# Kernel tuning notes

Measured on AMD Instinct MI355X. Metric: run time of the kernel, lower is better.

## Reference

```python
import jax, jax.numpy as jnp
import numpy as np

WS = 14           # window_size
N = WS * WS       # tokens = 196
DIM = 768
H = 12
HD = DIM // H     # 64
B = 256
KSZ = 3


def make_local_mask():
    # True = masked out; 3x3 neighborhood around each query is kept (False)
    mask = np.ones((N, N), dtype=bool)
    for i in range(WS):
        for j in range(WS):
            cur = np.ones((WS, WS), dtype=bool)
            stx, sty = max(i - KSZ // 2, 0), max(j - KSZ // 2, 0)
            edx, edy = min(i + KSZ // 2, WS - 1), min(j + KSZ // 2, WS - 1)
            cur[stx:edx + 1, sty:edy + 1] = False
            mask[i * WS + j] = cur.reshape(-1)
    return mask


def make_rel_idx():
    coords = np.stack(np.meshgrid(np.arange(WS), np.arange(WS), indexing='ij'))  # [2,WS,WS]
    flat = coords.reshape(2, -1)                                                  # [2,N]
    rel = flat[:, :, None] - flat[:, None, :]                                     # [2,N,N]
    rel = rel.transpose(1, 2, 0).astype(np.int32)                                 # [N,N,2]
    rel[:, :, 0] += WS - 1
    rel[:, :, 1] += WS - 1
    rel[:, :, 0] *= 2 * WS - 1
    return rel.sum(-1)                                                            # [N,N] in [0, (2WS-1)^2)


def setup_inputs() -> dict:
    key = jax.random.key(0)
    ks = jax.random.split(key, 5)
    return {
        'x': jax.random.normal(ks[0], (B, N, DIM), jnp.float32),
        'w_qkv': jax.random.normal(ks[1], (3 * DIM, DIM), jnp.float32) * 0.02,
        'rpb_table': jax.random.normal(ks[2], ((2 * WS - 1) ** 2, H), jnp.float32) * 0.02,
        'proj_w': jax.random.normal(ks[3], (DIM, DIM), jnp.float32) * 0.02,
        'proj_b': jax.random.normal(ks[4], (DIM,), jnp.float32) * 0.02,
        'mask': jnp.asarray(make_local_mask()),
        'rel_idx': jnp.asarray(make_rel_idx()),
    }


def reference(x, w_qkv, rpb_table, proj_w, proj_b, mask, rel_idx):
    b, n, c = x.shape
    scale = HD ** -0.5
    qkv = x @ w_qkv.T                                   # [B,N,3*DIM]
    qkv = qkv.reshape(b, n, 3, H, HD).transpose(2, 0, 3, 1, 4)  # [3,B,H,N,HD]
    q, k, v = qkv[0] * scale, qkv[1], qkv[2]
    attn = jnp.einsum('bhqd,bhkd->bhqk', q, k)          # [B,H,N,N]
    neg = -jnp.finfo(attn.dtype).max
    attn = jnp.where(mask, neg, attn)
    # relative position bias gather: [N,N] indices into [T,H] -> [H,N,N]
    rpb = rpb_table[rel_idx].transpose(2, 0, 1)
    attn = attn + rpb[None]
    attn = jax.nn.softmax(attn, axis=-1)
    out = jnp.einsum('bhqk,bhkd->bhqd', attn, v)        # [B,H,N,HD]
    out = out.transpose(0, 2, 1, 3).reshape(b, n, H * HD)
    return out @ proj_w.T + proj_b
```

## Files before the change

### kernel.cpp

```cpp
#include <hip/hip_runtime.h>
#include <cstdint>
#include <cstddef>

typedef unsigned short u16;
typedef __attribute__((ext_vector_type(8))) short bf16x8;
typedef __attribute__((ext_vector_type(4))) float f32x4;

__device__ __forceinline__ u16 f2bf(float f) {
    unsigned u = __float_as_uint(f);
    u += 0x7FFF + ((u >> 16) & 1);
    return (u16)(u >> 16);
}
__device__ __forceinline__ float bf2f(u16 b) {
    return __uint_as_float(((unsigned)b) << 16);
}

__global__ __launch_bounds__(256) void cvt_bf16(const float4* __restrict__ in,
                                                u16* __restrict__ out, int n4) {
    int i = blockIdx.x * 256 + threadIdx.x;
    if (i >= n4) return;
    float4 v = in[i];
    ushort4 o;
    o.x = f2bf(v.x); o.y = f2bf(v.y); o.z = f2bf(v.z); o.w = f2bf(v.w);
    ((ushort4*)out)[i] = o;
}

constexpr int BM = 128, BN = 128, BK = 32;

__device__ __forceinline__ void gl_lds16(const u16* g, u16* l) {
    __builtin_amdgcn_global_load_lds(
        (const __attribute__((address_space(1))) void*)g,
        (__attribute__((address_space(3))) void*)l, 16, 0, 0);
}

template <bool IS_QKV>
__global__ __launch_bounds__(256)
void gemm_bt(const u16* __restrict__ A, const u16* __restrict__ Bt,
             const float* __restrict__ bias, void* __restrict__ Cout,
             int M, int N, int K)
{
    __shared__ u16 As[BM * BK];
    __shared__ u16 Bs[BN * BK];

    const int tid  = threadIdx.x;
    const int wave = tid >> 6;
    const int lane = tid & 63;

    const int m0 = blockIdx.y * BM;
    const int n0 = blockIdx.x * BN;

    const int wm = (wave >> 1) * 64;
    const int wn = (wave & 1) * 64;

    const int fr = lane & 15;
    const int fks = (((lane >> 4) ^ ((fr >> 1) & 3)) * 8);

    f32x4 acc[4][4] = {};

    const int srow = wave * 32 + (lane >> 2);
    const int scol = (((lane & 3) ^ ((lane >> 3) & 3)) * 8);
    const u16* ag = A  + (size_t)(m0 + srow) * K + scol;
    const u16* bg = Bt + (size_t)(n0 + srow) * K + scol;
    u16* al0 = As + wave * 1024;
    u16* al1 = As + wave * 1024 + 512;
    u16* bl0 = Bs + wave * 1024;
    u16* bl1 = Bs + wave * 1024 + 512;

    for (int k0 = 0; k0 < K; k0 += BK) {
        gl_lds16(ag + k0,           al0);
        gl_lds16(ag + k0 + 16 * K,  al1);
        gl_lds16(bg + k0,           bl0);
        gl_lds16(bg + k0 + 16 * K,  bl1);
        __syncthreads();

        bf16x8 af[4], bfv[4];
        #pragma unroll
        for (int t = 0; t < 4; ++t) {
            af[t]  = *(const bf16x8*)(As + (wm + t * 16 + fr) * BK + fks);
            bfv[t] = *(const bf16x8*)(Bs + (wn + t * 16 + fr) * BK + fks);
        }
        #pragma unroll
        for (int tm = 0; tm < 4; ++tm)
            #pragma unroll
            for (int tn = 0; tn < 4; ++tn)
                acc[tm][tn] = __builtin_amdgcn_mfma_f32_16x16x32_bf16(
                    af[tm], bfv[tn], acc[tm][tn], 0, 0, 0);
        __syncthreads();
    }

    if (IS_QKV) {
        u16* C = (u16*)Cout;
        #pragma unroll
        for (int tm = 0; tm < 4; ++tm) {
            const int r0 = m0 + wm + tm * 16 + (lane >> 4) * 4;
            #pragma unroll
            for (int tn = 0; tn < 4; ++tn) {
                const int col = n0 + wn + tn * 16 + fr;
                const float sc = (col < 768) ? 0.125f : 1.0f;
                #pragma unroll
                for (int r = 0; r < 4; ++r)
                    C[(size_t)(r0 + r) * N + col] = f2bf(acc[tm][tn][r] * sc);
            }
        }
    } else {
        float* C = (float*)Cout;
        #pragma unroll
        for (int tm = 0; tm < 4; ++tm) {
            const int r0 = m0 + wm + tm * 16 + (lane >> 4) * 4;
            #pragma unroll
            for (int tn = 0; tn < 4; ++tn) {
                const int col = n0 + wn + tn * 16 + fr;
                const float b = bias[col];
                #pragma unroll
                for (int r = 0; r < 4; ++r)
                    C[(size_t)(r0 + r) * N + col] = acc[tm][tn][r] + b;
            }
        }
    }
}

__device__ __forceinline__ void load_bf8(const u16* p, float* f) {
    uint4 d = *(const uint4*)p;
    f[0] = __uint_as_float(d.x << 16); f[1] = __uint_as_float(d.x & 0xFFFF0000u);
    f[2] = __uint_as_float(d.y << 16); f[3] = __uint_as_float(d.y & 0xFFFF0000u);
    f[4] = __uint_as_float(d.z << 16); f[5] = __uint_as_float(d.z & 0xFFFF0000u);
    f[6] = __uint_as_float(d.w << 16); f[7] = __uint_as_float(d.w & 0xFFFF0000u);
}

__global__ __launch_bounds__(256)
void attn_sparse2(const u16* __restrict__ qkv, const float* __restrict__ rpb,
                  u16* __restrict__ out)
{
    const int lane = threadIdx.x & 63;
    const int wid  = blockIdx.x * 4 + (threadIdx.x >> 6);
    const int sub  = lane >> 3;
    const int sl   = lane & 7;
    const int gq   = wid * 8 + sub;
    const int bt   = gq / 12;
    const int h    = gq - bt * 12;
    const int t    = bt % 196;
    const int i    = t / 14, j = t % 14;

    const size_t rowbase = (size_t)(bt - t) * 2304 + h * 64 + sl * 8;

    float qf[8];
    load_bf8(qkv + (size_t)bt * 2304 + h * 64 + sl * 8, qf);

    float s[9];
    int   t2a[9];
    #pragma unroll
    for (int di = -1; di <= 1; ++di) {
        #pragma unroll
        for (int dj = -1; dj <= 1; ++dj) {
            const int idx = (di + 1) * 3 + (dj + 1);
            const int i2 = i + di, j2 = j + dj;
            const bool valid = ((unsigned)i2 < 14u) && ((unsigned)j2 < 14u);
            const int t2 = valid ? (i2 * 14 + j2) : t;
            t2a[idx] = t2;
            float kf[8];
            load_bf8(qkv + rowbase + (size_t)t2 * 2304 + 768, kf);
            float p = qf[0] * kf[0];
            #pragma unroll
            for (int d = 1; d < 8; ++d) p = fmaf(qf[d], kf[d], p);
            p += __shfl_xor(p, 1);
            p += __shfl_xor(p, 2);
            p += __shfl_xor(p, 4);
            const int ridx = (13 - di) * 27 + (13 - dj);
            s[idx] = valid ? (p + rpb[ridx * 12 + h]) : -1e30f;
        }
    }
    float mx = s[0];
    #pragma unroll
    for (int a = 1; a < 9; ++a) mx = fmaxf(mx, s[a]);

    float den = 0.f, o[8] = {};
    #pragma unroll
    for (int a = 0; a < 9; ++a) {
        float vf[8];
        load_bf8(qkv + rowbase + (size_t)t2a[a] * 2304 + 1536, vf);
        const float p = __expf(s[a] - mx);
        den += p;
        #pragma unroll
        for (int d = 0; d < 8; ++d) o[d] = fmaf(p, vf[d], o[d]);
    }
    const float r = 1.0f / den;
    ushort4 o0, o1;
    o0.x = f2bf(o[0] * r); o0.y = f2bf(o[1] * r);
    o0.z = f2bf(o[2] * r); o0.w = f2bf(o[3] * r);
    o1.x = f2bf(o[4] * r); o1.y = f2bf(o[5] * r);
    o1.z = f2bf(o[6] * r); o1.w = f2bf(o[7] * r);
    u16* op = out + (size_t)bt * 768 + h * 64 + sl * 8;
    *(ushort4*)op = o0;
    *(ushort4*)(op + 4) = o1;
}

extern "C" void kernel_launch(void* const* d_in, const int* in_sizes, int n_in,
                              void* d_out, int out_size, void* d_ws, size_t ws_size,
                              hipStream_t stream)
{
    const float* x      = (const float*)d_in[0];
    const float* w_qkv  = (const float*)d_in[1];
    const float* rpb    = (const float*)d_in[2];
    const float* proj_w = (const float*)d_in[3];
    const float* proj_b = (const float*)d_in[4];
    float* out = (float*)d_out;

    char* ws = (char*)d_ws;
    u16* x_bf    = (u16*)(ws);
    u16* wqkv_bf = (u16*)(ws + 77070336ULL);
    u16* pw_bf   = (u16*)(ws + 80609280ULL);
    u16* qkv_bf  = (u16*)(ws + 81788928ULL);
    u16* attn_bf = (u16*)(ws + 312999936ULL);

    cvt_bf16<<<37632, 256, 0, stream>>>((const float4*)x,      x_bf,    9633792);
    cvt_bf16<<<1728,  256, 0, stream>>>((const float4*)w_qkv,  wqkv_bf, 442368);
    cvt_bf16<<<576,   256, 0, stream>>>((const float4*)proj_w, pw_bf,   147456);

    gemm_bt<true><<<dim3(18, 392), 256, 0, stream>>>(
        x_bf, wqkv_bf, nullptr, qkv_bf, 50176, 2304, 768);

    attn_sparse2<<<18816, 256, 0, stream>>>(qkv_bf, rpb, attn_bf);

    gemm_bt<false><<<dim3(6, 392), 256, 0, stream>>>(
        attn_bf, pw_bf, proj_b, out, 50176, 768, 768);
}
```

Measured before the change: 756.4 us.

## Replace GEMM with 256x256 double-buffered pipelined MFMA kernel and XCD-aware tile remap

Swaps the 128x128 single-buffer GEMM for a 512-thread 256x256-tile kernel with BK=64 and double-buffered LDS. Global-to-LDS loads for the next k-step are interleaved with MFMA phases, and s_setprio raises priority during the MFMA runs. Block indices are remapped so neighbouring tiles land on the same XCD. The goal is to hide load latency and raise data reuse per tile, at the cost of more LDS and registers per block and fewer blocks in flight.

```diff
diff --git a/kernel.cpp b/kernel.cpp
--- a/kernel.cpp
+++ b/kernel.cpp
@@ -25,95 +25,174 @@
     ((ushort4*)out)[i] = o;
 }
 
-constexpr int BM = 128, BN = 128, BK = 32;
-
 __device__ __forceinline__ void gl_lds16(const u16* g, u16* l) {
     __builtin_amdgcn_global_load_lds(
         (const __attribute__((address_space(1))) void*)g,
         (__attribute__((address_space(3))) void*)l, 16, 0, 0);
 }
 
+#define MFMA16(a, b, c) __builtin_amdgcn_mfma_f32_16x16x32_bf16(a, b, c, 0, 0, 0)
+
+__device__ __forceinline__ void BARRIER() {
+    asm volatile("" ::: "memory");
+    __builtin_amdgcn_s_barrier();
+    asm volatile("" ::: "memory");
+}
+#define LGKM0() asm volatile("s_waitcnt lgkmcnt(0)" ::: "memory")
+
+__device__ __forceinline__ bf16x8 lds_frag(const u16* base, int r, int c) {
+    return *(const bf16x8*)((const char*)base + (r << 7) + ((c ^ (r & 7)) << 4));
+}
+
+__device__ __forceinline__ void stage_half(const u16* gbase, int K, u16* lbase,
+                                           int kt, int h, int srow, int wuoff)
+{
+    const u16* gp = gbase + (size_t)(h * 128 + srow) * K + kt * 64;
+    char* lp = (char*)lbase + h * 16384 + wuoff;
+    gl_lds16(gp, (u16*)lp);
+    gl_lds16(gp + (size_t)64 * K, (u16*)(lp + 8192));
+}
+
 template <bool IS_QKV>
-__global__ __launch_bounds__(256)
-void gemm_bt(const u16* __restrict__ A, const u16* __restrict__ Bt,
+__global__ __launch_bounds__(512, 2)
+void gemm256(const u16* __restrict__ A, const u16* __restrict__ Bt,
              const float* __restrict__ bias, void* __restrict__ Cout,
              int M, int N, int K)
 {
-    __shared__ u16 As[BM * BK];
-    __shared__ u16 Bs[BN * BK];
-
-    const int tid  = threadIdx.x;
-    const int wave = tid >> 6;
-    const int lane = tid & 63;
-
-    const int m0 = blockIdx.y * BM;
-    const int n0 = blockIdx.x * BN;
-
-    const int wm = (wave >> 1) * 64;
-    const int wn = (wave & 1) * 64;
-
-    const int fr = lane & 15;
-    const int fks = (((lane >> 4) ^ ((fr >> 1) & 3)) * 8);
-
-    f32x4 acc[4][4] = {};
-
-    const int srow = wave * 32 + (lane >> 2);
-    const int scol = (((lane & 3) ^ ((lane >> 3) & 3)) * 8);
-    const u16* ag = A  + (size_t)(m0 + srow) * K + scol;
-    const u16* bg = Bt + (size_t)(n0 + srow) * K + scol;
-    u16* al0 = As + wave * 1024;
-    u16* al1 = As + wave * 1024 + 512;
-    u16* bl0 = Bs + wave * 1024;
-    u16* bl1 = Bs + wave * 1024 + 512;
-
-    for (int k0 = 0; k0 < K; k0 += BK) {
-        gl_lds16(ag + k0,           al0);
-        gl_lds16(ag + k0 + 16 * K,  al1);
-        gl_lds16(bg + k0,           bl0);
-        gl_lds16(bg + k0 + 16 * K,  bl1);
-        __syncthreads();
-
-        bf16x8 af[4], bfv[4];
-        #pragma unroll
-        for (int t = 0; t < 4; ++t) {
-            af[t]  = *(const bf16x8*)(As + (wm + t * 16 + fr) * BK + fks);
-            bfv[t] = *(const bf16x8*)(Bs + (wn + t * 16 + fr) * BK + fks);
-        }
-        #pragma unroll
-        for (int tm = 0; tm < 4; ++tm)
-            #pragma unroll
-            for (int tn = 0; tn < 4; ++tn)
-                acc[tm][tn] = __builtin_amdgcn_mfma_f32_16x16x32_bf16(
-                    af[tm], bfv[tn], acc[tm][tn], 0, 0, 0);
-        __syncthreads();
+    __shared__ u16 As[2][16384];
+    __shared__ u16 Bs[2][16384];
+
+    const int tid = threadIdx.x;
+    const int w   = tid >> 6;
+    const int l   = tid & 63;
+    const int wr  = w >> 2;
+    const int wc  = w & 3;
+    const int fr  = l & 15;
+    const int ck0 = l >> 4;
+
+    const int gx = gridDim.x;
+    const int nwg = gx * gridDim.y;
+    const int orig = blockIdx.y * gx + blockIdx.x;
+    const int qq = nwg >> 3, rr = nwg & 7;
+    const int xcd = orig & 7, idx = orig >> 3;
+    const int wg = (xcd < rr) ? (xcd * (qq + 1) + idx)
+                              : (rr * (qq + 1) + (xcd - rr) * qq + idx);
+    const int bx = wg % gx, by = wg / gx;
+    const int m0 = by * 256, n0 = bx * 256;
+
+    const int srow   = w * 8 + (l >> 3);
+    const int schunk = ((l & 7) ^ (l >> 3)) * 8;
+    const int wuoff  = w * 1024;
+
+    const u16* Ag = A  + (size_t)m0 * K + schunk;
+    const u16* Bg = Bt + (size_t)n0 * K + schunk;
+
+    f32x4 acc[8][4] = {};
+    const int NT = K >> 6;
+
+    stage_half(Ag, K, As[0], 0, 0, srow, wuoff);
+    stage_half(Bg, K, Bs[0], 0, 0, srow, wuoff);
+    stage_half(Ag, K, As[0], 0, 1, srow, wuoff);
+    stage_half(Bg, K, Bs[0], 0, 1, srow, wuoff);
+    stage_half(Ag, K, As[1], 1, 0, srow, wuoff);
+    stage_half(Bg, K, Bs[1], 1, 0, srow, wuoff);
+    asm volatile("s_waitcnt vmcnt(4)" ::: "memory");
+    BARRIER();
+
+    for (int g = 0; g < NT; ++g) {
+        const u16* Ab = As[g & 1];
+        const u16* Bb = Bs[g & 1];
+        u16* Anx = As[(g + 1) & 1];
+        u16* Bnx = Bs[(g + 1) & 1];
+        u16* Acu = As[g & 1];
+        u16* Bcu = Bs[g & 1];
+
+        bf16x8 a0[8], a1[8], b0[4], b1[4];
+
+        #pragma unroll
+        for (int mi = 0; mi < 8; ++mi) a0[mi] = lds_frag(Ab, wr * 128 + mi * 16 + fr, ck0);
+        b0[0] = lds_frag(Bb, wc * 64 + 0 * 16 + fr, ck0);
+        b0[1] = lds_frag(Bb, wc * 64 + 1 * 16 + fr, ck0);
+        if (g + 1 < NT) stage_half(Ag, K, Anx, g + 1, 1, srow, wuoff);
+        BARRIER();
+        LGKM0();
+        __builtin_amdgcn_s_setprio(1);
+        #pragma unroll
+        for (int mi = 0; mi < 8; ++mi) {
+            acc[mi][0] = MFMA16(a0[mi], b0[0], acc[mi][0]);
+            acc[mi][1] = MFMA16(a0[mi], b0[1], acc[mi][1]);
+        }
+        __builtin_amdgcn_s_setprio(0);
+        BARRIER();
+
+        b0[2] = lds_frag(Bb, wc * 64 + 2 * 16 + fr, ck0);
+        b0[3] = lds_frag(Bb, wc * 64 + 3 * 16 + fr, ck0);
+        #pragma unroll
+        for (int mi = 0; mi < 8; ++mi) a1[mi] = lds_frag(Ab, wr * 128 + mi * 16 + fr, ck0 + 4);
+        #pragma unroll
+        for (int ni = 0; ni < 4; ++ni) b1[ni] = lds_frag(Bb, wc * 64 + ni * 16 + fr, ck0 + 4);
+        if (g + 1 < NT) stage_half(Bg, K, Bnx, g + 1, 1, srow, wuoff);
+        BARRIER();
+        LGKM0();
+        __builtin_amdgcn_s_setprio(1);
+        #pragma unroll
+        for (int mi = 0; mi < 8; ++mi) {
+            acc[mi][2] = MFMA16(a0[mi], b0[2], acc[mi][2]);
+            acc[mi][3] = MFMA16(a0[mi], b0[3], acc[mi][3]);
+        }
+        __builtin_amdgcn_s_setprio(0);
+        BARRIER();
+
+        if (g + 2 < NT) stage_half(Ag, K, Acu, g + 2, 0, srow, wuoff);
+        BARRIER();
+        __builtin_amdgcn_s_setprio(1);
+        #pragma unroll
+        for (int mi = 0; mi < 8; ++mi) {
+            acc[mi][0] = MFMA16(a1[mi], b1[0], acc[mi][0]);
+            acc[mi][1] = MFMA16(a1[mi], b1[1], acc[mi][1]);
+        }
+        __builtin_amdgcn_s_setprio(0);
+        BARRIER();
+
+        if (g + 2 < NT) stage_half(Bg, K, Bcu, g + 2, 0, srow, wuoff);
+        __builtin_amdgcn_s_setprio(1);
+        #pragma unroll
+        for (int mi = 0; mi < 8; ++mi) {
+            acc[mi][2] = MFMA16(a1[mi], b1[2], acc[mi][2]);
+            acc[mi][3] = MFMA16(a1[mi], b1[3], acc[mi][3]);
+        }
+        __builtin_amdgcn_s_setprio(0);
+        if (g < NT - 2) { asm volatile("s_waitcnt vmcnt(4)" ::: "memory"); }
+        else            { asm volatile("s_waitcnt vmcnt(0)" ::: "memory"); }
+        BARRIER();
     }
 
     if (IS_QKV) {
         u16* C = (u16*)Cout;
         #pragma unroll
-        for (int tm = 0; tm < 4; ++tm) {
-            const int r0 = m0 + wm + tm * 16 + (lane >> 4) * 4;
+        for (int mi = 0; mi < 8; ++mi) {
+            const int r0 = m0 + wr * 128 + mi * 16 + (l >> 4) * 4;
             #pragma unroll
-            for (int tn = 0; tn < 4; ++tn) {
-                const int col = n0 + wn + tn * 16 + fr;
+            for (int ni = 0; ni < 4; ++ni) {
+                const int col = n0 + wc * 64 + ni * 16 + fr;
                 const float sc = (col < 768) ? 0.125f : 1.0f;
                 #pragma unroll
                 for (int r = 0; r < 4; ++r)
-                    C[(size_t)(r0 + r) * N + col] = f2bf(acc[tm][tn][r] * sc);
+                    C[(size_t)(r0 + r) * N + col] = f2bf(acc[mi][ni][r] * sc);
             }
         }
     } else {
         float* C = (float*)Cout;
         #pragma unroll
-        for (int tm = 0; tm < 4; ++tm) {
-            const int r0 = m0 + wm + tm * 16 + (lane >> 4) * 4;
+        for (int mi = 0; mi < 8; ++mi) {
+            const int r0 = m0 + wr * 128 + mi * 16 + (l >> 4) * 4;
             #pragma unroll
-            for (int tn = 0; tn < 4; ++tn) {
-                const int col = n0 + wn + tn * 16 + fr;
+            for (int ni = 0; ni < 4; ++ni) {
+                const int col = n0 + wc * 64 + ni * 16 + fr;
                 const float b = bias[col];
                 #pragma unroll
                 for (int r = 0; r < 4; ++r)
-                    C[(size_t)(r0 + r) * N + col] = acc[tm][tn][r] + b;
+                    C[(size_t)(r0 + r) * N + col] = acc[mi][ni][r] + b;
             }
         }
     }
@@ -216,11 +295,11 @@
     cvt_bf16<<<1728,  256, 0, stream>>>((const float4*)w_qkv,  wqkv_bf, 442368);
     cvt_bf16<<<576,   256, 0, stream>>>((const float4*)proj_w, pw_bf,   147456);
 
-    gemm_bt<true><<<dim3(18, 392), 256, 0, stream>>>(
+    gemm256<true><<<dim3(9, 196), 512, 0, stream>>>(
         x_bf, wqkv_bf, nullptr, qkv_bf, 50176, 2304, 768);
 
     attn_sparse2<<<18816, 256, 0, stream>>>(qkv_bf, rpb, attn_bf);
 
-    gemm_bt<false><<<dim3(6, 392), 256, 0, stream>>>(
+    gemm256<false><<<dim3(3, 196), 512, 0, stream>>>(
         attn_bf, pw_bf, proj_b, out, 50176, 768, 768);
 }
```

Result: faster. 703.6 us (-7.0%).
